# Kernel tuning notes

Hardware: AMD Instinct MI355X
Metric: run time of the kernel (lower is better)

The kernel has to match this reference:

```python
import jax, jax.numpy as jnp
import numpy as np

LENGTHSCALE = 0.3
EPS = 1e-10
N = 100000   # evaluation points
M = 3375     # grid_size**3 RBF centers


def setup_inputs() -> dict:
    key = jax.random.key(0)
    k1, k2, k3, k4, k5 = jax.random.split(key, 5)
    x = jax.random.normal(k1, (N, 3), dtype=jnp.float32)
    centers = jax.random.normal(k2, (M, 3), dtype=jnp.float32)
    coeff_u = jax.random.normal(k3, (M,), dtype=jnp.float32)
    coeff_v = jax.random.normal(k4, (M,), dtype=jnp.float32)
    coeff_w = jax.random.normal(k5, (M,), dtype=jnp.float32)
    return {"x": x, "centers": centers, "coeff_u": coeff_u,
            "coeff_v": coeff_v, "coeff_w": coeff_w}


def reference(x, centers, coeff_u, coeff_v, coeff_w):
    # base sphere-attractor field: x * (1 - ||x||)
    r = jnp.linalg.norm(x, axis=-1, keepdims=True)          # (N, 1)
    base = x * (1.0 - r)                                    # (N, 3)

    x_sq = jnp.sum(x * x, axis=-1, keepdims=True)           # (N, 1)
    c_sq = jnp.sum(centers * centers, axis=-1)[None, :]     # (1, M)
    xy = x @ centers.T                                      # (N, M)
    dist2 = jnp.maximum(x_sq + c_sq - 2.0 * xy, EPS)        # (N, M)

    # RBF features and three shared-phi matvecs fused as one matmul
    phi = jnp.exp(-dist2 / (2.0 * LENGTHSCALE ** 2))        # (N, M)
    coeffs = jnp.stack([coeff_u, coeff_v, coeff_w], axis=1) # (M, 3)
    uvw = phi @ coeffs                                      # (N, 3)
    return base + uvw
```

## Files before the change

### kernel.cpp

```cpp
#include <hip/hip_runtime.h>

#define S2 8.014973f
#define K2 16.029946f
#define ONEB ((unsigned short)0x3F80)
#define PT 4
#define BW 4

typedef float f32x4 __attribute__((ext_vector_type(4)));
typedef short bf16x8 __attribute__((ext_vector_type(8)));

__device__ __forceinline__ unsigned short bhi(float v) {
    unsigned int b = __builtin_bit_cast(unsigned int, v);
    return (unsigned short)((b + 0x7FFFu + ((b >> 16) & 1u)) >> 16);
}
__device__ __forceinline__ float bf2f(unsigned short h) {
    unsigned int u = ((unsigned int)h) << 16;
    return __builtin_bit_cast(float, u);
}

__global__ void rbf_prep(const float* __restrict__ centers,
                         const float* __restrict__ cu,
                         const float* __restrict__ cv,
                         const float* __restrict__ cw,
                         uint4* __restrict__ afrag,
                         float* __restrict__ bpack, int M) {
    const int T = blockIdx.x;
    const int lane = threadIdx.x;
    const int row = lane & 15, g = lane >> 4;
    const int c = T * 16 + row;
    float cx = 0.f, cy = 0.f, cz = 0.f;
    if (c < M) { cx = centers[3*c]; cy = centers[3*c+1]; cz = centers[3*c+2]; }
    const float a1 = K2 * cx, a2 = K2 * cy, a3 = K2 * cz;
    const float a4 = -S2 * (cx*cx + cy*cy + cz*cz);
    const unsigned short a1h = bhi(a1), a2h = bhi(a2), a3h = bhi(a3), a4h = bhi(a4);
    const unsigned short a1l = bhi(a1 - bf2f(a1h));
    const unsigned short a2l = bhi(a2 - bf2f(a2h));
    const unsigned short a3l = bhi(a3 - bf2f(a3h));
    const unsigned short a4l = bhi(a4 - bf2f(a4h));
    const unsigned short F[16] = {a1h, a1h, a1l, a2h, a2h, a2l, a3h, a3h,
                                  a3l, a4h, a4l, ONEB, ONEB, 0, 0, 0};
    uint4 u;
    u.x = (unsigned int)F[8*g+0] | ((unsigned int)F[8*g+1] << 16);
    u.y = (unsigned int)F[8*g+2] | ((unsigned int)F[8*g+3] << 16);
    u.z = (unsigned int)F[8*g+4] | ((unsigned int)F[8*g+5] << 16);
    u.w = (unsigned int)F[8*g+6] | ((unsigned int)F[8*g+7] << 16);
    afrag[T * 64 + lane] = u;

    if (lane < 48) {
        const int g2 = lane / 12, idx = lane % 12;
        const int comp = idx >> 2, r = idx & 3;
        const int c2 = T * 16 + g2 * 4 + r;
        float v = 0.f;
        if (c2 < M)
            v = (comp == 0) ? cu[c2] : ((comp == 1) ? cv[c2] : cw[c2]);
        bpack[(T * 12 + g2 * 3 + comp) * 4 + r] = v;
    }
}

__global__ __launch_bounds__(256) void rbf_main(
        const float* __restrict__ x,
        const uint4* __restrict__ afrag,
        const float4* __restrict__ bpack4,
        float* __restrict__ out, int N, int NT) {
    __shared__ float acc[BW][64][3];

    const int tid = threadIdx.x;
    const int lane = tid & 63;
    const int w = __builtin_amdgcn_readfirstlane(tid >> 6);
    const int col = lane & 15, g = lane >> 4;
    const int pb = blockIdx.x * (16 * PT);

    float xx[PT], xy[PT], xz[PT];
    bf16x8 bfrag[PT];
#pragma unroll
    for (int t = 0; t < PT; ++t) {
        const int p = pb + t * 16 + col;
        float a0 = 0.f, a1 = 0.f, a2 = 0.f;
        if (p < N) { a0 = x[3*p]; a1 = x[3*p+1]; a2 = x[3*p+2]; }
        xx[t] = a0; xy[t] = a1; xz[t] = a2;
        const float px = -S2 * (a0*a0 + a1*a1 + a2*a2);
        const unsigned short xh = bhi(a0), yh = bhi(a1), zh = bhi(a2);
        const unsigned short xl = bhi(a0 - bf2f(xh));
        const unsigned short yl = bhi(a1 - bf2f(yh));
        const unsigned short zl = bhi(a2 - bf2f(zh));
        const unsigned short ph = bhi(px), pl = bhi(px - bf2f(ph));
        unsigned int b0 = 0, b1 = 0, b2 = 0, b3 = 0;
        if (g == 0) {
            b0 = (unsigned int)xh | ((unsigned int)xl << 16);
            b1 = (unsigned int)xh | ((unsigned int)yh << 16);
            b2 = (unsigned int)yl | ((unsigned int)yh << 16);
            b3 = (unsigned int)zh | ((unsigned int)zl << 16);
        } else if (g == 1) {
            b0 = (unsigned int)zh | ((unsigned int)ONEB << 16);
            b1 = (unsigned int)ONEB | ((unsigned int)ph << 16);
            b2 = (unsigned int)pl;
            b3 = 0;
        }
        uint4 bu_;
        bu_.x = b0; bu_.y = b1; bu_.z = b2; bu_.w = b3;
        bfrag[t] = __builtin_bit_cast(bf16x8, bu_);
    }

    const f32x4 zero = {0.f, 0.f, 0.f, 0.f};
    float au[PT], av[PT], aw[PT];
#pragma unroll
    for (int t = 0; t < PT; ++t) { au[t] = 0.f; av[t] = 0.f; aw[t] = 0.f; }

    const uint4* __restrict__ ap = afrag + lane;
    const float4* __restrict__ bp = bpack4 + g * 3;

    const int per = (NT + BW - 1) / BW;
    const int jb = w * per;
    const int je = min(jb + per, NT);

#pragma unroll 2
    for (int T = jb; T < je; ++T) {
        const uint4 a = ap[T * 64];
        const float4 bu = bp[T * 12 + 0];
        const float4 bv = bp[T * 12 + 1];
        const float4 bw = bp[T * 12 + 2];
        const bf16x8 af = __builtin_bit_cast(bf16x8, a);
#pragma unroll
        for (int t = 0; t < PT; ++t) {
            const f32x4 E = __builtin_amdgcn_mfma_f32_16x16x32_bf16(
                af, bfrag[t], zero, 0, 0, 0);
            const float p0 = __builtin_amdgcn_exp2f(E[0]);
            const float p1 = __builtin_amdgcn_exp2f(E[1]);
            const float p2 = __builtin_amdgcn_exp2f(E[2]);
            const float p3 = __builtin_amdgcn_exp2f(E[3]);
            au[t] = fmaf(p0, bu.x, au[t]); au[t] = fmaf(p1, bu.y, au[t]);
            au[t] = fmaf(p2, bu.z, au[t]); au[t] = fmaf(p3, bu.w, au[t]);
            av[t] = fmaf(p0, bv.x, av[t]); av[t] = fmaf(p1, bv.y, av[t]);
            av[t] = fmaf(p2, bv.z, av[t]); av[t] = fmaf(p3, bv.w, av[t]);
            aw[t] = fmaf(p0, bw.x, aw[t]); aw[t] = fmaf(p1, bw.y, aw[t]);
            aw[t] = fmaf(p2, bw.z, aw[t]); aw[t] = fmaf(p3, bw.w, aw[t]);
        }
    }

#pragma unroll
    for (int t = 0; t < PT; ++t) {
        au[t] += __shfl_xor(au[t], 16); au[t] += __shfl_xor(au[t], 32);
        av[t] += __shfl_xor(av[t], 16); av[t] += __shfl_xor(av[t], 32);
        aw[t] += __shfl_xor(aw[t], 16); aw[t] += __shfl_xor(aw[t], 32);
    }

    if (w == 0 && g == 0) {
#pragma unroll
        for (int t = 0; t < PT; ++t) {
            const float r = sqrtf(xx[t]*xx[t] + xy[t]*xy[t] + xz[t]*xz[t]);
            const float s = 1.f - r;
            au[t] = fmaf(xx[t], s, au[t]);
            av[t] = fmaf(xy[t], s, av[t]);
            aw[t] = fmaf(xz[t], s, aw[t]);
        }
    }

    if (g == 0) {
#pragma unroll
        for (int t = 0; t < PT; ++t) {
            acc[w][t * 16 + col][0] = au[t];
            acc[w][t * 16 + col][1] = av[t];
            acc[w][t * 16 + col][2] = aw[t];
        }
    }
    __syncthreads();

    if (tid < 192) {
        const int gi = pb * 3 + tid;
        if (gi < 3 * N) {
            const int pl = tid / 3, c = tid % 3;
            float s = acc[0][pl][c] + acc[1][pl][c] +
                      acc[2][pl][c] + acc[3][pl][c];
            out[gi] = s;
        }
    }
}

extern "C" void kernel_launch(void* const* d_in, const int* in_sizes, int n_in,
                              void* d_out, int out_size, void* d_ws,
                              size_t ws_size, hipStream_t stream) {
    const float* x = (const float*)d_in[0];
    const float* centers = (const float*)d_in[1];
    const float* cu = (const float*)d_in[2];
    const float* cv = (const float*)d_in[3];
    const float* cw = (const float*)d_in[4];
    float* out = (float*)d_out;
    const int N = in_sizes[0] / 3;
    const int M = in_sizes[1] / 3;
    const int NT = (M + 15) / 16;

    uint4* afrag = (uint4*)d_ws;
    float* bpack = (float*)((char*)d_ws + (size_t)NT * 1024);

    hipLaunchKernelGGL(rbf_prep, dim3(NT), dim3(64), 0, stream,
                       centers, cu, cv, cw, afrag, bpack, M);
    hipLaunchKernelGGL(rbf_main, dim3((N + 16 * PT - 1) / (16 * PT)),
                       dim3(256), 0, stream,
                       x, afrag, (const float4*)bpack, out, N, NT);
}
```

Baseline: 133.1 us.

## Halve points per block, prefetch next tile, and use packed float2 FMAs

Cuts points per block from 64 to 32, which doubles the grid and gives more blocks to spread across CUs. The center loop now loads the next tile's A-fragment and coefficients while computing the current one, hiding load latency. The per-tile coefficient FMAs are regrouped into float2 vector operations so the compiler can emit packed FMA instructions. The cost is that each block reloads the full center table over half as many points, so global and L2 traffic per point doubles, and the loop runs without unrolling.

```diff
diff --git a/kernel.cpp b/kernel.cpp
--- a/kernel.cpp
+++ b/kernel.cpp
@@ -3,10 +3,11 @@
 #define S2 8.014973f
 #define K2 16.029946f
 #define ONEB ((unsigned short)0x3F80)
-#define PT 4
-#define BW 4
+#define PT 2
+#define NW 4
 
 typedef float f32x4 __attribute__((ext_vector_type(4)));
+typedef float f2 __attribute__((ext_vector_type(2)));
 typedef short bf16x8 __attribute__((ext_vector_type(8)));
 
 __device__ __forceinline__ unsigned short bhi(float v) {
@@ -62,7 +63,7 @@
         const uint4* __restrict__ afrag,
         const float4* __restrict__ bpack4,
         float* __restrict__ out, int N, int NT) {
-    __shared__ float acc[BW][64][3];
+    __shared__ float acc[NW][32][3];
 
     const int tid = threadIdx.x;
     const int lane = tid & 63;
@@ -102,43 +103,58 @@
     }
 
     const f32x4 zero = {0.f, 0.f, 0.f, 0.f};
-    float au[PT], av[PT], aw[PT];
-#pragma unroll
-    for (int t = 0; t < PT; ++t) { au[t] = 0.f; av[t] = 0.f; aw[t] = 0.f; }
+    f2 AU[PT], AV[PT], AW[PT];
+#pragma unroll
+    for (int t = 0; t < PT; ++t) {
+        AU[t] = (f2){0.f, 0.f}; AV[t] = (f2){0.f, 0.f}; AW[t] = (f2){0.f, 0.f};
+    }
 
     const uint4* __restrict__ ap = afrag + lane;
     const float4* __restrict__ bp = bpack4 + g * 3;
 
-    const int per = (NT + BW - 1) / BW;
+    const int per = (NT + NW - 1) / NW;
     const int jb = w * per;
     const int je = min(jb + per, NT);
 
-#pragma unroll 2
-    for (int T = jb; T < je; ++T) {
-        const uint4 a = ap[T * 64];
-        const float4 bu = bp[T * 12 + 0];
-        const float4 bv = bp[T * 12 + 1];
-        const float4 bw = bp[T * 12 + 2];
-        const bf16x8 af = __builtin_bit_cast(bf16x8, a);
-#pragma unroll
-        for (int t = 0; t < PT; ++t) {
-            const f32x4 E = __builtin_amdgcn_mfma_f32_16x16x32_bf16(
-                af, bfrag[t], zero, 0, 0, 0);
-            const float p0 = __builtin_amdgcn_exp2f(E[0]);
-            const float p1 = __builtin_amdgcn_exp2f(E[1]);
-            const float p2 = __builtin_amdgcn_exp2f(E[2]);
-            const float p3 = __builtin_amdgcn_exp2f(E[3]);
-            au[t] = fmaf(p0, bu.x, au[t]); au[t] = fmaf(p1, bu.y, au[t]);
-            au[t] = fmaf(p2, bu.z, au[t]); au[t] = fmaf(p3, bu.w, au[t]);
-            av[t] = fmaf(p0, bv.x, av[t]); av[t] = fmaf(p1, bv.y, av[t]);
-            av[t] = fmaf(p2, bv.z, av[t]); av[t] = fmaf(p3, bv.w, av[t]);
-            aw[t] = fmaf(p0, bw.x, aw[t]); aw[t] = fmaf(p1, bw.y, aw[t]);
-            aw[t] = fmaf(p2, bw.z, aw[t]); aw[t] = fmaf(p3, bw.w, aw[t]);
-        }
-    }
-
+    if (jb < je) {
+        uint4 a_c = ap[jb * 64];
+        float4 bu_c = bp[jb * 12 + 0];
+        float4 bv_c = bp[jb * 12 + 1];
+        float4 bw_c = bp[jb * 12 + 2];
+        for (int T = jb; T < je; ++T) {
+            const int Tn = (T + 1 < je) ? T + 1 : T;
+            const uint4 a_n = ap[Tn * 64];
+            const float4 bu_n = bp[Tn * 12 + 0];
+            const float4 bv_n = bp[Tn * 12 + 1];
+            const float4 bw_n = bp[Tn * 12 + 2];
+
+            const bf16x8 af = __builtin_bit_cast(bf16x8, a_c);
+            const f2 BU01 = {bu_c.x, bu_c.y}, BU23 = {bu_c.z, bu_c.w};
+            const f2 BV01 = {bv_c.x, bv_c.y}, BV23 = {bv_c.z, bv_c.w};
+            const f2 BW01 = {bw_c.x, bw_c.y}, BW23 = {bw_c.z, bw_c.w};
+#pragma unroll
+            for (int t = 0; t < PT; ++t) {
+                const f32x4 E = __builtin_amdgcn_mfma_f32_16x16x32_bf16(
+                    af, bfrag[t], zero, 0, 0, 0);
+                f2 P01, P23;
+                P01.x = __builtin_amdgcn_exp2f(E[0]);
+                P01.y = __builtin_amdgcn_exp2f(E[1]);
+                P23.x = __builtin_amdgcn_exp2f(E[2]);
+                P23.y = __builtin_amdgcn_exp2f(E[3]);
+                AU[t] += P01 * BU01; AU[t] += P23 * BU23;
+                AV[t] += P01 * BV01; AV[t] += P23 * BV23;
+                AW[t] += P01 * BW01; AW[t] += P23 * BW23;
+            }
+            a_c = a_n; bu_c = bu_n; bv_c = bv_n; bw_c = bw_n;
+        }
+    }
+
+    float au[PT], av[PT], aw[PT];
 #pragma unroll
     for (int t = 0; t < PT; ++t) {
+        au[t] = AU[t].x + AU[t].y;
+        av[t] = AV[t].x + AV[t].y;
+        aw[t] = AW[t].x + AW[t].y;
         au[t] += __shfl_xor(au[t], 16); au[t] += __shfl_xor(au[t], 32);
         av[t] += __shfl_xor(av[t], 16); av[t] += __shfl_xor(av[t], 32);
         aw[t] += __shfl_xor(aw[t], 16); aw[t] += __shfl_xor(aw[t], 32);
@@ -165,13 +181,12 @@
     }
     __syncthreads();
 
-    if (tid < 192) {
+    if (tid < 96) {
         const int gi = pb * 3 + tid;
         if (gi < 3 * N) {
             const int pl = tid / 3, c = tid % 3;
-            float s = acc[0][pl][c] + acc[1][pl][c] +
+            out[gi] = acc[0][pl][c] + acc[1][pl][c] +
                       acc[2][pl][c] + acc[3][pl][c];
-            out[gi] = s;
         }
     }
 }
```

After: 146.8 us. +10.3%, slower.
